# Optimization experiments

Hardware: AMD Instinct MI355X
Metric: run time of the kernel (lower is better)

## Reference

```python
import jax, jax.numpy as jnp
import numpy as np

H = 4
N = 1024
E = 4096
LE = 16384
FN = 128
FE = 64
FNO = 128
FEO = 64


def _lin(x, W, b):
    # torch nn.Linear: y = x @ W.T + b, W is [out, in]
    return x @ W.T + b


def setup_inputs() -> dict:
    key = jax.random.key(0)
    ks = jax.random.split(key, 24)
    s = 0.05
    inp = {}
    inp["node_inputs"] = jax.random.normal(ks[0], (N, FN), jnp.float32)
    inp["edge_inputs"] = jax.random.normal(ks[1], (E, FE), jnp.float32)
    inp["src"] = jax.random.randint(ks[2], (E,), 0, N, jnp.int32)
    inp["dst"] = jax.random.randint(ks[3], (E,), 0, N, jnp.int32)
    inp["lg_src"] = jax.random.randint(ks[4], (LE,), 0, E, jnp.int32)
    inp["lg_dst"] = jax.random.randint(ks[5], (LE,), 0, E, jnp.int32)
    # projection linear weights (torch Linear layout [out, in])
    inp["nqW"] = jax.random.normal(ks[6], (H * FN, FN), jnp.float32) * s
    inp["nqb"] = jax.random.normal(ks[7], (H * FN,), jnp.float32) * s
    inp["nkW"] = jax.random.normal(ks[8], (H, FN), jnp.float32) * s
    inp["nkb"] = jax.random.normal(ks[9], (H,), jnp.float32) * s
    inp["nvW"] = jax.random.normal(ks[10], (H * FN, FN), jnp.float32) * s
    inp["nvb"] = jax.random.normal(ks[11], (H * FN,), jnp.float32) * s
    inp["eqW"] = jax.random.normal(ks[12], (H * FE, FE), jnp.float32) * s
    inp["eqb"] = jax.random.normal(ks[13], (H * FE,), jnp.float32) * s
    inp["ekW"] = jax.random.normal(ks[14], (H, FE), jnp.float32) * s
    inp["ekb"] = jax.random.normal(ks[15], (H,), jnp.float32) * s
    inp["evW"] = jax.random.normal(ks[16], (H * FE, FE), jnp.float32) * s
    inp["evb"] = jax.random.normal(ks[17], (H * FE,), jnp.float32) * s
    # convolution output linears
    inp["ncW"] = jax.random.normal(ks[18], (FNO, FN), jnp.float32) * s
    inp["ncb"] = jax.random.normal(ks[19], (FNO,), jnp.float32) * s
    inp["ecW"] = jax.random.normal(ks[20], (FEO, FE), jnp.float32) * s
    inp["ecb"] = jax.random.normal(ks[21], (FEO,), jnp.float32) * s
    return inp


def reference(node_inputs, edge_inputs, src, dst, lg_src, lg_dst,
              nqW, nqb, nkW, nkb, nvW, nvb,
              eqW, eqb, ekW, ekb, evW, evb,
              ncW, ncb, ecW, ecb):
    n, fn = node_inputs.shape
    e, fe = edge_inputs.shape
    # per-head Q/K/V projections; .view(H, -1, F) == row-major reshape
    nq = _lin(node_inputs, nqW, nqb).reshape(H, -1, fn)   # [H,N,FN]
    nk = _lin(node_inputs, nkW, nkb).reshape(H, -1, 1)    # [H,N,1]
    nv = _lin(node_inputs, nvW, nvb).reshape(H, -1, fn)   # [H,N,FN]
    eq = _lin(edge_inputs, eqW, eqb).reshape(H, -1, fe)   # [H,E,FE]
    ek = _lin(edge_inputs, ekW, ekb).reshape(H, -1, 1)    # [H,E,1]
    ev = _lin(edge_inputs, evW, evb).reshape(H, -1, fe)   # [H,E,FE]
    # self attention: softmax(Q @ Q^T @ K, dim=1); associate as Q @ (Q^T K)
    node_sa = jax.nn.softmax(nq @ (jnp.swapaxes(nq, -1, -2) @ nk), axis=1)  # [H,N,1]
    edge_sa = jax.nn.softmax(eq @ (jnp.swapaxes(eq, -1, -2) @ ek), axis=1)  # [H,E,1]
    # vectorized edge-indexed scatter of attention scores into dense projections
    node_proj = jnp.zeros((H, n, n), node_inputs.dtype).at[:, src, dst].set(edge_sa[:, :, 0])
    conn = dst[lg_src]  # g.find_edges(source)[1]: destination node of edge lg_src
    edge_proj = jnp.zeros((H, e, e), edge_inputs.dtype).at[:, lg_src, lg_dst].set(node_sa[:, conn, 0])
    # dense adjacency matrices
    A = jnp.zeros((n, n), node_inputs.dtype).at[src, dst].set(1.0)
    Alg = jnp.zeros((e, e), edge_inputs.dtype).at[lg_src, lg_dst].set(1.0)
    # 'sum' aggregation: (attn_proj * A) @ value, then Linear + relu
    node_out = jax.nn.relu(_lin((node_proj * A) @ nv, ncW, ncb))   # [H,N,FNO]
    edge_out = jax.nn.relu(_lin((edge_proj * Alg) @ ev, ecW, ecb)) # [H,E,FEO]
    return (node_out, edge_out)
```

## Files before the change

kernel.cpp:

```cpp
#include <hip/hip_runtime.h>

#define H_ 4
#define N_ 1024
#define E_ 4096
#define LE_ 16384
#define FN_ 128
#define FE_ 64
#define CAP_ 32

struct P {
  const float *Xn, *Xe;
  const int *src, *dst, *lgs, *lgd;
  const float *nqW, *nqb, *nkW, *nkb, *nvW, *nvb;
  const float *eqW, *eqb, *ekW, *ekb, *evW, *evb;
  const float *ncW, *ncb, *ecW, *ecb;
  float *out;
  float *NV, *EV, *nsa, *esa, *nagg, *eagg;
  int *cntN, *cntE, *listN, *listE;
};

template<int K, bool RELU>
__device__ void gemm_tile(const float* __restrict__ X, const float* __restrict__ W,
                          const float* __restrict__ b, float* __restrict__ C,
                          int O, int r0, int o0, float* smem, int t) {
  float* Xs = smem;
  float* Ws = smem + 2048;
  const int tn = t & 15, tm = t >> 4;
  float acc[4][4] = {};
  for (int k0 = 0; k0 < K; k0 += 32) {
#pragma unroll
    for (int ph = 0; ph < 2; ++ph) {
      int i4 = t + ph * 256;
      int m = i4 >> 3;
      int k4 = (i4 & 7) << 2;
      int m4 = m >> 2, ml = m & 3;
      float4 vx = *(const float4*)&X[(r0 + m) * K + k0 + k4];
      float4 vw = *(const float4*)&W[(o0 + m) * K + k0 + k4];
      Xs[(k4 + 0) * 64 + ((m4 ^ ((k4 + 0) & 15)) << 2) + ml] = vx.x;
      Xs[(k4 + 1) * 64 + ((m4 ^ ((k4 + 1) & 15)) << 2) + ml] = vx.y;
      Xs[(k4 + 2) * 64 + ((m4 ^ ((k4 + 2) & 15)) << 2) + ml] = vx.z;
      Xs[(k4 + 3) * 64 + ((m4 ^ ((k4 + 3) & 15)) << 2) + ml] = vx.w;
      Ws[(k4 + 0) * 64 + ((m4 ^ ((k4 + 0) & 15)) << 2) + ml] = vw.x;
      Ws[(k4 + 1) * 64 + ((m4 ^ ((k4 + 1) & 15)) << 2) + ml] = vw.y;
      Ws[(k4 + 2) * 64 + ((m4 ^ ((k4 + 2) & 15)) << 2) + ml] = vw.z;
      Ws[(k4 + 3) * 64 + ((m4 ^ ((k4 + 3) & 15)) << 2) + ml] = vw.w;
    }
    __syncthreads();
#pragma unroll
    for (int k = 0; k < 32; ++k) {
      float4 a = *(const float4*)&Xs[k * 64 + ((tm ^ (k & 15)) << 2)];
      float4 b4 = *(const float4*)&Ws[k * 64 + ((tn ^ (k & 15)) << 2)];
      acc[0][0] += a.x * b4.x; acc[0][1] += a.x * b4.y; acc[0][2] += a.x * b4.z; acc[0][3] += a.x * b4.w;
      acc[1][0] += a.y * b4.x; acc[1][1] += a.y * b4.y; acc[1][2] += a.y * b4.z; acc[1][3] += a.y * b4.w;
      acc[2][0] += a.z * b4.x; acc[2][1] += a.z * b4.y; acc[2][2] += a.z * b4.z; acc[2][3] += a.z * b4.w;
      acc[3][0] += a.w * b4.x; acc[3][1] += a.w * b4.y; acc[3][2] += a.w * b4.z; acc[3][3] += a.w * b4.w;
    }
    __syncthreads();
  }
  float4 bv = *(const float4*)&b[o0 + tn * 4];
#pragma unroll
  for (int i = 0; i < 4; ++i) {
    float4 o;
    o.x = acc[i][0] + bv.x; o.y = acc[i][1] + bv.y;
    o.z = acc[i][2] + bv.z; o.w = acc[i][3] + bv.w;
    if (RELU) {
      o.x = fmaxf(o.x, 0.f); o.y = fmaxf(o.y, 0.f);
      o.z = fmaxf(o.z, 0.f); o.w = fmaxf(o.w, 0.f);
    }
    *(float4*)&C[(r0 + tm * 4 + i) * O + o0 + tn * 4] = o;
  }
}

__global__ __launch_bounds__(1024) void kA(P p) {
  __shared__ float S[16384];
  const int tid = threadIdx.x, bid = blockIdx.x;

  if (bid < 96) {
    int st = tid >> 8, tt = tid & 255;
    float* sm = S + st * 4096;
    if (bid < 32) {
      int T = bid * 4 + st;
      gemm_tile<128, false>(p.Xn, p.nvW, p.nvb, p.NV, 512, (T >> 3) * 64, (T & 7) * 64, sm, tt);
    } else {
      int T2 = (bid - 32) * 4 + st;
      gemm_tile<64, false>(p.Xe, p.evW, p.evb, p.EV, 256, (T2 >> 2) * 64, (T2 & 3) * 64, sm, tt);
    }
    return;
  }
  if (bid >= 104) {
    int idx = (bid - 104) * 1024 + tid;
    if (idx < E_) {
      int e = idx, s = p.src[e], d = p.dst[e];
      int pos = atomicAdd(&p.cntN[s], 1);
      p.listN[s * CAP_ + ((unsigned)pos & (CAP_ - 1))] = (d << 12) | e;
    } else {
      int l = idx - E_, j = p.lgs[l], c = p.lgd[l];
      int pos = atomicAdd(&p.cntE[j], 1);
      p.listE[j * CAP_ + ((unsigned)pos & (CAP_ - 1))] = (c << 14) | l;
    }
    return;
  }

  float4* accs = (float4*)S;
  float* sc    = S + 4096;
  float* knel  = S + 8192;
  float* red   = S + 12288;
  float* ys    = S + 13312;
  float* ts    = S + 13824;
  float* zs    = S + 13952;
  float* ds    = S + 14480;
  float* sig   = S + 14484;

  if (bid < 100) {
    const int h = bid - 96;
    const int r0 = h * 256;
    {
      int rl = tid >> 2, c = tid & 3;
      const float4* x4 = (const float4*)(p.Xn + (r0 + rl) * FN_);
      const float4* w4 = (const float4*)(p.nkW + c * FN_);
      float acc = p.nkb[c];
      for (int k = 0; k < 32; ++k) {
        float4 x = x4[k], w = w4[k];
        acc += x.x * w.x + x.y * w.y + x.z * w.z + x.w * w.w;
      }
      knel[rl * 4 + c] = acc;
    }
    __syncthreads();
    {
      int g = tid & 127, q = tid >> 7;
      float a0 = 0, a1 = 0, a2 = 0, a3 = 0;
      for (int jj = 0; jj < 32; ++jj) {
        int rl = q * 32 + jj;
        float x = p.Xn[(r0 + rl) * FN_ + g];
        float4 k = ((float4*)knel)[rl];
        a0 += x * k.x; a1 += x * k.y; a2 += x * k.z; a3 += x * k.w;
      }
      accs[tid] = make_float4(a0, a1, a2, a3);
    }
    __syncthreads();
    for (int off = 512; off >= 128; off >>= 1) {
      if (tid < off) {
        float4 a = accs[tid], b = accs[tid + off];
        accs[tid] = make_float4(a.x + b.x, a.y + b.y, a.z + b.z, a.w + b.w);
      }
      __syncthreads();
    }
    if (tid < 128) {
      float4 a = accs[tid];
      ys[tid * 4 + 0] = a.x; ys[tid * 4 + 1] = a.y;
      ys[tid * 4 + 2] = a.z; ys[tid * 4 + 3] = a.w;
    }
    if (tid >= 128 && tid < 160) {
      int t2 = tid - 128, c = t2 & 3, part = t2 >> 2;
      float s = 0.f;
      for (int j = 0; j < 32; ++j) s += knel[(part * 32 + j) * 4 + c];
      red[t2] = s;
    }
    __syncthreads();
    if (tid < 4) { float s = 0.f; for (int q = 0; q < 8; ++q) s += red[q * 4 + tid]; sig[tid] = s; }
    __syncthreads();
    if (tid < 512) {
      const float4* w4 = (const float4*)(p.nqW + tid * FN_);
      int c = tid >> 7;
      float s = 0.f;
      for (int g4 = 0; g4 < 32; ++g4) {
        float4 w = w4[g4];
        s += w.x * ys[(g4 * 4 + 0) * 4 + c] + w.y * ys[(g4 * 4 + 1) * 4 + c]
           + w.z * ys[(g4 * 4 + 2) * 4 + c] + w.w * ys[(g4 * 4 + 3) * 4 + c];
      }
      red[tid] = s;
    }
    __syncthreads();
    if (tid < 128) {
      float s = red[tid] + red[128 + tid] + red[256 + tid] + red[384 + tid];
      float bb = 0.f;
      for (int c = 0; c < 4; ++c) bb += p.nqb[c * 128 + tid] * sig[c];
      ts[tid] = s + bb;
    }
    __syncthreads();
    if (tid < 512) {
      int c = tid >> 7, g = tid & 127;
      float s = 0.f;
      for (int f = 0; f < 128; ++f) s += p.nqW[(c * 128 + f) * 128 + g] * ts[f];
      zs[c * 132 + g] = s;
    }
    if (tid >= 512 && tid < 516) {
      int c = tid - 512;
      float s = 0.f;
      for (int f = 0; f < 128; ++f) s += p.nqb[c * 128 + f] * ts[f];
      ds[c] = s;
    }
    __syncthreads();
    float scv;
    {
      int c = tid & 3, j = tid >> 2;
      const float4* x4 = (const float4*)(p.Xn + (r0 + j) * FN_);
      const float* z = zs + c * 132;
      float s = ds[c];
      for (int g4 = 0; g4 < 32; ++g4) {
        float4 x = x4[g4];
        s += x.x * z[g4 * 4] + x.y * z[g4 * 4 + 1] + x.z * z[g4 * 4 + 2] + x.w * z[g4 * 4 + 3];
      }
      scv = s;
    }
    red[tid] = scv;
    __syncthreads();
    for (int off = 512; off > 0; off >>= 1) {
      if (tid < off) red[tid] = fmaxf(red[tid], red[tid + off]);
      __syncthreads();
    }
    float m = red[0];
    __syncthreads();
    float e = expf(scv - m);
    red[tid] = e;
    __syncthreads();
    for (int off = 512; off > 0; off >>= 1) {
      if (tid < off) red[tid] += red[tid + off];
      __syncthreads();
    }
    p.nsa[h * N_ + tid] = e / red[0];
  } else {
    const int h = bid - 100;
    const int r0 = h * 1024;
    {
      const float4* x4 = (const float4*)(p.Xe + (r0 + tid) * FE_);
      const float4* w0 = (const float4*)(p.ekW + 0 * FE_);
      const float4* w1 = (const float4*)(p.ekW + 1 * FE_);
      const float4* w2 = (const float4*)(p.ekW + 2 * FE_);
      const float4* w3 = (const float4*)(p.ekW + 3 * FE_);
      float a0 = p.ekb[0], a1 = p.ekb[1], a2 = p.ekb[2], a3 = p.ekb[3];
      for (int k = 0; k < 16; ++k) {
        float4 x = x4[k];
        float4 u0 = w0[k], u1 = w1[k], u2 = w2[k], u3 = w3[k];
        a0 += x.x * u0.x + x.y * u0.y + x.z * u0.z + x.w * u0.w;
        a1 += x.x * u1.x + x.y * u1.y + x.z * u1.z + x.w * u1.w;
        a2 += x.x * u2.x + x.y * u2.y + x.z * u2.z + x.w * u2.w;
        a3 += x.x * u3.x + x.y * u3.y + x.z * u3.z + x.w * u3.w;
      }
      ((float4*)knel)[tid] = make_float4(a0, a1, a2, a3);
    }
    __syncthreads();
    {
      int g = tid & 63, q = tid >> 6;
      float a0 = 0, a1 = 0, a2 = 0, a3 = 0;
      for (int jj = 0; jj < 64; ++jj) {
        int rl = q * 64 + jj;
        float x = p.Xe[(r0 + rl) * FE_ + g];
        float4 k = ((float4*)knel)[rl];
        a0 += x * k.x; a1 += x * k.y; a2 += x * k.z; a3 += x * k.w;
      }
      accs[tid] = make_float4(a0, a1, a2, a3);
    }
    __syncthreads();
    for (int off = 512; off >= 64; off >>= 1) {
      if (tid < off) {
        float4 a = accs[tid], b = accs[tid + off];
        accs[tid] = make_float4(a.x + b.x, a.y + b.y, a.z + b.z, a.w + b.w);
      }
      __syncthreads();
    }
    if (tid < 64) {
      float4 a = accs[tid];
      ys[tid * 4 + 0] = a.x; ys[tid * 4 + 1] = a.y;
      ys[tid * 4 + 2] = a.z; ys[tid * 4 + 3] = a.w;
    }
    if (tid >= 128 && tid < 160) {
      int t2 = tid - 128, c = t2 & 3, part = t2 >> 2;
      float s = 0.f;
      for (int j = 0; j < 128; ++j) s += knel[(part * 128 + j) * 4 + c];
      red[t2] = s;
    }
    __syncthreads();
    if (tid < 4) { float s = 0.f; for (int q = 0; q < 8; ++q) s += red[q * 4 + tid]; sig[tid] = s; }
    __syncthreads();
    if (tid < 256) {
      const float4* w4 = (const float4*)(p.eqW + tid * FE_);
      int c = tid >> 6;
      float s = 0.f;
      for (int g4 = 0; g4 < 16; ++g4) {
        float4 w = w4[g4];
        s += w.x * ys[(g4 * 4 + 0) * 4 + c] + w.y * ys[(g4 * 4 + 1) * 4 + c]
           + w.z * ys[(g4 * 4 + 2) * 4 + c] + w.w * ys[(g4 * 4 + 3) * 4 + c];
      }
      red[tid] = s;
    }
    __syncthreads();
    if (tid < 64) {
      float s = red[tid] + red[64 + tid] + red[128 + tid] + red[192 + tid];
      float bb = 0.f;
      for (int c = 0; c < 4; ++c) bb += p.eqb[c * 64 + tid] * sig[c];
      ts[tid] = s + bb;
    }
    __syncthreads();
    if (tid < 256) {
      int c = tid >> 6, g = tid & 63;
      float s = 0.f;
      for (int f = 0; f < 64; ++f) s += p.eqW[(c * 64 + f) * 64 + g] * ts[f];
      zs[c * 132 + g] = s;
    }
    if (tid >= 256 && tid < 260) {
      int c = tid - 256;
      float s = 0.f;
      for (int f = 0; f < 64; ++f) s += p.eqb[c * 64 + f] * ts[f];
      ds[c] = s;
    }
    __syncthreads();
    float s4[4];
    {
      const float4* x4 = (const float4*)(p.Xe + (r0 + tid) * FE_);
      s4[0] = ds[0]; s4[1] = ds[1]; s4[2] = ds[2]; s4[3] = ds[3];
      for (int g4 = 0; g4 < 16; ++g4) {
        float4 x = x4[g4];
#pragma unroll
        for (int c = 0; c < 4; ++c) {
          const float* z = zs + c * 132 + g4 * 4;
          s4[c] += x.x * z[0] + x.y * z[1] + x.z * z[2] + x.w * z[3];
        }
      }
    }
    float lm = fmaxf(fmaxf(s4[0], s4[1]), fmaxf(s4[2], s4[3]));
    red[tid] = lm;
    __syncthreads();
    for (int off = 512; off > 0; off >>= 1) {
      if (tid < off) red[tid] = fmaxf(red[tid], red[tid + off]);
      __syncthreads();
    }
    float m = red[0];
    __syncthreads();
    float e0 = expf(s4[0] - m), e1 = expf(s4[1] - m);
    float e2 = expf(s4[2] - m), e3 = expf(s4[3] - m);
    red[tid] = e0 + e1 + e2 + e3;
    __syncthreads();
    for (int off = 512; off > 0; off >>= 1) {
      if (tid < off) red[tid] += red[tid + off];
      __syncthreads();
    }
    float inv = 1.f / red[0];
    ((float4*)(p.esa + h * E_))[tid] = make_float4(e0 * inv, e1 * inv, e2 * inv, e3 * inv);
  }
}

__global__ __launch_bounds__(256) void kB_gather(P p) {
  int idx = blockIdx.x * 256 + threadIdx.x;
  if (idx < N_ * 32) {
    unsigned base = (unsigned)p.cntN[N_];
    int s = idx >> 5, f4 = idx & 31;
    int deg = min((int)((unsigned)p.cntN[s] - base), CAP_);
    const int* lst = p.listN + s * CAP_;
    float4 acc[H_];
#pragma unroll
    for (int h = 0; h < H_; ++h) acc[h] = make_float4(0.f, 0.f, 0.f, 0.f);
    for (int i = 0; i < deg; ++i) {
      int pk = lst[(base + i) & (CAP_ - 1)];
      int d = pk >> 12, e = pk & (E_ - 1);
      bool win = true;
      for (int k = 0; k < deg; ++k) {
        int pk2 = lst[(base + k) & (CAP_ - 1)];
        if ((pk2 >> 12) == d && pk2 > pk) win = false;
      }
      if (!win) continue;
#pragma unroll
      for (int h = 0; h < H_; ++h) {
        float a = p.esa[h * E_ + e];
        float4 v = ((const float4*)(p.NV + h * (N_ * FN_) + d * FN_))[f4];
        acc[h].x += a * v.x; acc[h].y += a * v.y;
        acc[h].z += a * v.z; acc[h].w += a * v.w;
      }
    }
#pragma unroll
    for (int h = 0; h < H_; ++h)
      ((float4*)(p.nagg + h * (N_ * FN_) + s * FN_))[f4] = acc[h];
  } else {
    idx -= N_ * 32;
    unsigned base = (unsigned)p.cntE[E_];
    int j = idx >> 4, f4 = idx & 15;
    int deg = min((int)((unsigned)p.cntE[j] - base), CAP_);
    const int* lst = p.listE + j * CAP_;
    float4 acc[H_];
#pragma unroll
    for (int h = 0; h < H_; ++h) acc[h] = make_float4(0.f, 0.f, 0.f, 0.f);
    for (int i = 0; i < deg; ++i) {
      int pk = lst[(base + i) & (CAP_ - 1)];
      int c = pk >> 14;
      bool win = true;
      for (int k = 0; k < deg; ++k) {
        int pk2 = lst[(base + k) & (CAP_ - 1)];
        if ((pk2 >> 14) == c && pk2 > pk) win = false;
      }
      if (!win) continue;
#pragma unroll
      for (int h = 0; h < H_; ++h) {
        float4 v = ((const float4*)(p.EV + h * (E_ * FE_) + c * FE_))[f4];
        acc[h].x += v.x; acc[h].y += v.y; acc[h].z += v.z; acc[h].w += v.w;
      }
    }
    int cn = p.dst[j];
#pragma unroll
    for (int h = 0; h < H_; ++h) {
      float a = p.nsa[h * N_ + cn];
      ((float4*)(p.eagg + h * (E_ * FE_) + j * FE_))[f4] =
          make_float4(a * acc[h].x, a * acc[h].y, a * acc[h].z, a * acc[h].w);
    }
  }
}

__global__ __launch_bounds__(256) void kC_out(P p) {
  __shared__ float smem[4096];
  const int t = threadIdx.x, bid = blockIdx.x;
  if (bid < 128)
    gemm_tile<128, true>(p.nagg, p.ncW, p.ncb, p.out, 128, (bid >> 1) * 64, (bid & 1) * 64, smem, t);
  else {
    int T2 = bid - 128;
    gemm_tile<64, true>(p.eagg, p.ecW, p.ecb, p.out + (size_t)H_ * N_ * 128, 64, T2 * 64, 0, smem, t);
  }
}

extern "C" void kernel_launch(void* const* d_in, const int* in_sizes, int n_in,
                              void* d_out, int out_size, void* d_ws, size_t ws_size,
                              hipStream_t stream) {
  P p;
  p.Xn  = (const float*)d_in[0];
  p.Xe  = (const float*)d_in[1];
  p.src = (const int*)d_in[2];
  p.dst = (const int*)d_in[3];
  p.lgs = (const int*)d_in[4];
  p.lgd = (const int*)d_in[5];
  p.nqW = (const float*)d_in[6];  p.nqb = (const float*)d_in[7];
  p.nkW = (const float*)d_in[8];  p.nkb = (const float*)d_in[9];
  p.nvW = (const float*)d_in[10]; p.nvb = (const float*)d_in[11];
  p.eqW = (const float*)d_in[12]; p.eqb = (const float*)d_in[13];
  p.ekW = (const float*)d_in[14]; p.ekb = (const float*)d_in[15];
  p.evW = (const float*)d_in[16]; p.evb = (const float*)d_in[17];
  p.ncW = (const float*)d_in[18]; p.ncb = (const float*)d_in[19];
  p.ecW = (const float*)d_in[20]; p.ecb = (const float*)d_in[21];
  p.out = (float*)d_out;

  float* f = (float*)d_ws;
  p.NV   = f; f += N_ * H_ * FN_;
  p.EV   = f; f += E_ * H_ * FE_;
  p.nsa  = f; f += H_ * N_;
  p.esa  = f; f += H_ * E_;
  p.nagg = f; f += H_ * N_ * FN_;
  p.eagg = f; f += H_ * E_ * FE_;
  p.cntN = (int*)f; f += N_ + 1;
  p.cntE = (int*)f; f += E_ + 1;
  p.listN = (int*)f; f += N_ * CAP_;
  p.listE = (int*)f; f += E_ * CAP_;

  kA<<<124, 1024, 0, stream>>>(p);
  kB_gather<<<384, 256, 0, stream>>>(p);
  kC_out<<<384, 256, 0, stream>>>(p);
}
```

Baseline: 185.2 us.

## Fuse sparse gather into output GEMM and precompute deduplicated adjacency lists

The aggregation step that wrote nagg/eagg to global memory is folded into the output-linear kernel. Each block now gathers its 64 rows straight into shared memory and runs the GEMM from there, which removes an intermediate write and read. The O(deg^2) duplicate-edge resolution now runs once per row into compacted lists, instead of once per feature lane. The V projections move out of the attention kernel into a separate 256-thread kernel with more blocks. In exchange, the gather in the output kernel has each thread hold 32 accumulators and read uncoalesced rows, which may hurt occupancy, and a one-thread-per-row dedup pass is added.

Result: faster. 180.6 us (-2.5%).

```diff
diff --git a/kernel.cpp b/kernel.cpp
--- a/kernel.cpp
+++ b/kernel.cpp
@@ -15,8 +15,11 @@
   const float *eqW, *eqb, *ekW, *ekb, *evW, *evb;
   const float *ncW, *ncb, *ecW, *ecb;
   float *out;
-  float *NV, *EV, *nsa, *esa, *nagg, *eagg;
-  int *cntN, *cntE, *listN, *listE;
+  float *NV, *EV, *nsa, *esa;
+  int *cntN, *cntE;
+  int *listN, *listE;
+  int *listNc, *listEc;
+  int *degN, *degE;
 };
 
 template<int K, bool RELU>
@@ -71,24 +74,12 @@
   }
 }
 
-__global__ __launch_bounds__(1024) void kA(P p) {
+__global__ __launch_bounds__(1024) void A_attn(P p) {
   __shared__ float S[16384];
   const int tid = threadIdx.x, bid = blockIdx.x;
 
-  if (bid < 96) {
-    int st = tid >> 8, tt = tid & 255;
-    float* sm = S + st * 4096;
-    if (bid < 32) {
-      int T = bid * 4 + st;
-      gemm_tile<128, false>(p.Xn, p.nvW, p.nvb, p.NV, 512, (T >> 3) * 64, (T & 7) * 64, sm, tt);
-    } else {
-      int T2 = (bid - 32) * 4 + st;
-      gemm_tile<64, false>(p.Xe, p.evW, p.evb, p.EV, 256, (T2 >> 2) * 64, (T2 & 3) * 64, sm, tt);
-    }
-    return;
-  }
-  if (bid >= 104) {
-    int idx = (bid - 104) * 1024 + tid;
+  if (bid >= 8) {
+    int idx = (bid - 8) * 1024 + tid;
     if (idx < E_) {
       int e = idx, s = p.src[e], d = p.dst[e];
       int pos = atomicAdd(&p.cntN[s], 1);
@@ -111,8 +102,8 @@
   float* ds    = S + 14480;
   float* sig   = S + 14484;
 
-  if (bid < 100) {
-    const int h = bid - 96;
+  if (bid < 4) {
+    const int h = bid;
     const int r0 = h * 256;
     {
       int rl = tid >> 2, c = tid & 3;
@@ -220,14 +211,14 @@
     }
     p.nsa[h * N_ + tid] = e / red[0];
   } else {
-    const int h = bid - 100;
+    const int h = bid - 4;
     const int r0 = h * 1024;
     {
       const float4* x4 = (const float4*)(p.Xe + (r0 + tid) * FE_);
-      const float4* w0 = (const float4*)(p.ekW + 0 * FE_);
-      const float4* w1 = (const float4*)(p.ekW + 1 * FE_);
-      const float4* w2 = (const float4*)(p.ekW + 2 * FE_);
-      const float4* w3 = (const float4*)(p.ekW + 3 * FE_);
+      const float4* w0 = (const float4*)(p.ekW);
+      const float4* w1 = (const float4*)(p.ekW + 64);
+      const float4* w2 = (const float4*)(p.ekW + 128);
+      const float4* w3 = (const float4*)(p.ekW + 192);
       float a0 = p.ekb[0], a1 = p.ekb[1], a2 = p.ekb[2], a3 = p.ekb[3];
       for (int k = 0; k < 16; ++k) {
         float4 x = x4[k];
@@ -340,78 +331,192 @@
   }
 }
 
-__global__ __launch_bounds__(256) void kB_gather(P p) {
-  int idx = blockIdx.x * 256 + threadIdx.x;
-  if (idx < N_ * 32) {
-    unsigned base = (unsigned)p.cntN[N_];
-    int s = idx >> 5, f4 = idx & 31;
-    int deg = min((int)((unsigned)p.cntN[s] - base), CAP_);
-    const int* lst = p.listN + s * CAP_;
-    float4 acc[H_];
-#pragma unroll
-    for (int h = 0; h < H_; ++h) acc[h] = make_float4(0.f, 0.f, 0.f, 0.f);
-    for (int i = 0; i < deg; ++i) {
-      int pk = lst[(base + i) & (CAP_ - 1)];
-      int d = pk >> 12, e = pk & (E_ - 1);
-      bool win = true;
-      for (int k = 0; k < deg; ++k) {
-        int pk2 = lst[(base + k) & (CAP_ - 1)];
-        if ((pk2 >> 12) == d && pk2 > pk) win = false;
-      }
-      if (!win) continue;
-#pragma unroll
-      for (int h = 0; h < H_; ++h) {
-        float a = p.esa[h * E_ + e];
-        float4 v = ((const float4*)(p.NV + h * (N_ * FN_) + d * FN_))[f4];
-        acc[h].x += a * v.x; acc[h].y += a * v.y;
-        acc[h].z += a * v.z; acc[h].w += a * v.w;
-      }
-    }
-#pragma unroll
-    for (int h = 0; h < H_; ++h)
-      ((float4*)(p.nagg + h * (N_ * FN_) + s * FN_))[f4] = acc[h];
+__global__ __launch_bounds__(256) void B_vproj(P p) {
+  __shared__ float S[4096];
+  const int t = threadIdx.x, bid = blockIdx.x;
+  if (bid < 128) {
+    gemm_tile<128, false>(p.Xn, p.nvW, p.nvb, p.NV, 512, (bid >> 3) * 64, (bid & 7) * 64, S, t);
+  } else if (bid < 384) {
+    int T2 = bid - 128;
+    gemm_tile<64, false>(p.Xe, p.evW, p.evb, p.EV, 256, (T2 >> 2) * 64, (T2 & 3) * 64, S, t);
   } else {
-    idx -= N_ * 32;
-    unsigned base = (unsigned)p.cntE[E_];
-    int j = idx >> 4, f4 = idx & 15;
-    int deg = min((int)((unsigned)p.cntE[j] - base), CAP_);
-    const int* lst = p.listE + j * CAP_;
-    float4 acc[H_];
-#pragma unroll
-    for (int h = 0; h < H_; ++h) acc[h] = make_float4(0.f, 0.f, 0.f, 0.f);
-    for (int i = 0; i < deg; ++i) {
-      int pk = lst[(base + i) & (CAP_ - 1)];
-      int c = pk >> 14;
-      bool win = true;
-      for (int k = 0; k < deg; ++k) {
-        int pk2 = lst[(base + k) & (CAP_ - 1)];
-        if ((pk2 >> 14) == c && pk2 > pk) win = false;
-      }
-      if (!win) continue;
-#pragma unroll
-      for (int h = 0; h < H_; ++h) {
-        float4 v = ((const float4*)(p.EV + h * (E_ * FE_) + c * FE_))[f4];
-        acc[h].x += v.x; acc[h].y += v.y; acc[h].z += v.z; acc[h].w += v.w;
-      }
-    }
-    int cn = p.dst[j];
-#pragma unroll
-    for (int h = 0; h < H_; ++h) {
-      float a = p.nsa[h * N_ + cn];
-      ((float4*)(p.eagg + h * (E_ * FE_) + j * FE_))[f4] =
-          make_float4(a * acc[h].x, a * acc[h].y, a * acc[h].z, a * acc[h].w);
+    int idx = (bid - 384) * 256 + t;
+    if (idx < N_) {
+      int s = idx;
+      unsigned base = (unsigned)p.cntN[N_];
+      int deg = min((int)((unsigned)p.cntN[s] - base), CAP_);
+      const int* lst = p.listN + s * CAP_;
+      int* dstl = p.listNc + s * CAP_;
+      int w = 0;
+      for (int i = 0; i < deg; ++i) {
+        int pk = lst[(base + i) & (CAP_ - 1)];
+        bool win = true;
+        for (int k2 = 0; k2 < deg; ++k2) {
+          int pk2 = lst[(base + k2) & (CAP_ - 1)];
+          if ((pk2 >> 12) == (pk >> 12) && pk2 > pk) win = false;
+        }
+        if (win) dstl[w++] = pk;
+      }
+      p.degN[s] = w;
+    } else {
+      int j = idx - N_;
+      unsigned base = (unsigned)p.cntE[E_];
+      int deg = min((int)((unsigned)p.cntE[j] - base), CAP_);
+      const int* lst = p.listE + j * CAP_;
+      int* dstl = p.listEc + j * CAP_;
+      int w = 0;
+      for (int i = 0; i < deg; ++i) {
+        int pk = lst[(base + i) & (CAP_ - 1)];
+        bool win = true;
+        for (int k2 = 0; k2 < deg; ++k2) {
+          int pk2 = lst[(base + k2) & (CAP_ - 1)];
+          if ((pk2 >> 14) == (pk >> 14) && pk2 > pk) win = false;
+        }
+        if (win) dstl[w++] = pk;
+      }
+      p.degE[j] = w;
     }
   }
 }
 
-__global__ __launch_bounds__(256) void kC_out(P p) {
-  __shared__ float smem[4096];
+__global__ __launch_bounds__(256) void C_out(P p) {
+  __shared__ float S[10240];
   const int t = threadIdx.x, bid = blockIdx.x;
-  if (bid < 128)
-    gemm_tile<128, true>(p.nagg, p.ncW, p.ncb, p.out, 128, (bid >> 1) * 64, (bid & 1) * 64, smem, t);
-  else {
-    int T2 = bid - 128;
-    gemm_tile<64, true>(p.eagg, p.ecW, p.ecb, p.out + (size_t)H_ * N_ * 128, 64, T2 * 64, 0, smem, t);
+  const int tn = t & 15, tm = t >> 4;
+  float* Xs = S;
+
+  if (bid < 128) {
+    float* Ws = S + 8192;
+    int rt = bid >> 1, o0 = (bid & 1) * 64;
+    int r0 = rt * 64;
+    int h = r0 >> 10, s0 = r0 & (N_ - 1);
+    {
+      int m = t >> 2, g0 = (t & 3) * 32;
+      int m4 = m >> 2, ml = m & 3;
+      int s = s0 + m;
+      int deg = p.degN[s];
+      const int* lst = p.listNc + s * CAP_;
+      float acc[32];
+#pragma unroll
+      for (int c = 0; c < 32; ++c) acc[c] = 0.f;
+      for (int i = 0; i < deg; ++i) {
+        int pk = lst[i];
+        int e = pk & (E_ - 1), d = pk >> 12;
+        float a = p.esa[h * E_ + e];
+        const float4* v4 = (const float4*)(p.NV + h * (N_ * FN_) + d * FN_ + g0);
+#pragma unroll
+        for (int c4 = 0; c4 < 8; ++c4) {
+          float4 v = v4[c4];
+          acc[c4 * 4 + 0] += a * v.x; acc[c4 * 4 + 1] += a * v.y;
+          acc[c4 * 4 + 2] += a * v.z; acc[c4 * 4 + 3] += a * v.w;
+        }
+      }
+#pragma unroll
+      for (int c = 0; c < 32; ++c) {
+        int k = g0 + c;
+        Xs[k * 64 + ((m4 ^ (k & 15)) << 2) + ml] = acc[c];
+      }
+    }
+    float accO[4][4] = {};
+    for (int k0 = 0; k0 < 128; k0 += 32) {
+      __syncthreads();
+#pragma unroll
+      for (int ph = 0; ph < 2; ++ph) {
+        int i4 = t + ph * 256;
+        int m = i4 >> 3, k4 = (i4 & 7) << 2;
+        int m4 = m >> 2, ml = m & 3;
+        float4 vw = *(const float4*)&p.ncW[(o0 + m) * 128 + k0 + k4];
+        Ws[(k4 + 0) * 64 + ((m4 ^ ((k4 + 0) & 15)) << 2) + ml] = vw.x;
+        Ws[(k4 + 1) * 64 + ((m4 ^ ((k4 + 1) & 15)) << 2) + ml] = vw.y;
+        Ws[(k4 + 2) * 64 + ((m4 ^ ((k4 + 2) & 15)) << 2) + ml] = vw.z;
+        Ws[(k4 + 3) * 64 + ((m4 ^ ((k4 + 3) & 15)) << 2) + ml] = vw.w;
+      }
+      __syncthreads();
+#pragma unroll
+      for (int k = 0; k < 32; ++k) {
+        int ka = k0 + k;
+        float4 a = *(const float4*)&Xs[ka * 64 + ((tm ^ (ka & 15)) << 2)];
+        float4 b4 = *(const float4*)&Ws[k * 64 + ((tn ^ (k & 15)) << 2)];
+        accO[0][0] += a.x * b4.x; accO[0][1] += a.x * b4.y; accO[0][2] += a.x * b4.z; accO[0][3] += a.x * b4.w;
+        accO[1][0] += a.y * b4.x; accO[1][1] += a.y * b4.y; accO[1][2] += a.y * b4.z; accO[1][3] += a.y * b4.w;
+        accO[2][0] += a.z * b4.x; accO[2][1] += a.z * b4.y; accO[2][2] += a.z * b4.z; accO[2][3] += a.z * b4.w;
+        accO[3][0] += a.w * b4.x; accO[3][1] += a.w * b4.y; accO[3][2] += a.w * b4.z; accO[3][3] += a.w * b4.w;
+      }
+    }
+    float4 bv = *(const float4*)&p.ncb[o0 + tn * 4];
+#pragma unroll
+    for (int i = 0; i < 4; ++i) {
+      float4 o;
+      o.x = fmaxf(accO[i][0] + bv.x, 0.f); o.y = fmaxf(accO[i][1] + bv.y, 0.f);
+      o.z = fmaxf(accO[i][2] + bv.z, 0.f); o.w = fmaxf(accO[i][3] + bv.w, 0.f);
+      *(float4*)&p.out[(r0 + tm * 4 + i) * 128 + o0 + tn * 4] = o;
+    }
+  } else {
+    float* Ws = S + 4096;
+    int T = bid - 128;
+    int r0 = T * 64;
+    int h = r0 >> 12, j0 = r0 & (E_ - 1);
+    {
+      int m = t >> 2, g0 = (t & 3) * 16;
+      int m4 = m >> 2, ml = m & 3;
+      int j = j0 + m;
+      int deg = p.degE[j];
+      const int* lst = p.listEc + j * CAP_;
+      float acc[16];
+#pragma unroll
+      for (int c = 0; c < 16; ++c) acc[c] = 0.f;
+      for (int i = 0; i < deg; ++i) {
+        int c = lst[i] >> 14;
+        const float4* v4 = (const float4*)(p.EV + h * (E_ * FE_) + c * FE_ + g0);
+#pragma unroll
+        for (int c4 = 0; c4 < 4; ++c4) {
+          float4 v = v4[c4];
+          acc[c4 * 4 + 0] += v.x; acc[c4 * 4 + 1] += v.y;
+          acc[c4 * 4 + 2] += v.z; acc[c4 * 4 + 3] += v.w;
+        }
+      }
+      float a = p.nsa[h * N_ + p.dst[j]];
+#pragma unroll
+      for (int c = 0; c < 16; ++c) {
+        int k = g0 + c;
+        Xs[k * 64 + ((m4 ^ (k & 15)) << 2) + ml] = a * acc[c];
+      }
+    }
+    float accO[4][4] = {};
+    for (int k0 = 0; k0 < 64; k0 += 32) {
+      __syncthreads();
+#pragma unroll
+      for (int ph = 0; ph < 2; ++ph) {
+        int i4 = t + ph * 256;
+        int m = i4 >> 3, k4 = (i4 & 7) << 2;
+        int m4 = m >> 2, ml = m & 3;
+        float4 vw = *(const float4*)&p.ecW[m * 64 + k0 + k4];
+        Ws[(k4 + 0) * 64 + ((m4 ^ ((k4 + 0) & 15)) << 2) + ml] = vw.x;
+        Ws[(k4 + 1) * 64 + ((m4 ^ ((k4 + 1) & 15)) << 2) + ml] = vw.y;
+        Ws[(k4 + 2) * 64 + ((m4 ^ ((k4 + 2) & 15)) << 2) + ml] = vw.z;
+        Ws[(k4 + 3) * 64 + ((m4 ^ ((k4 + 3) & 15)) << 2) + ml] = vw.w;
+      }
+      __syncthreads();
+#pragma unroll
+      for (int k = 0; k < 32; ++k) {
+        int ka = k0 + k;
+        float4 a = *(const float4*)&Xs[ka * 64 + ((tm ^ (ka & 15)) << 2)];
+        float4 b4 = *(const float4*)&Ws[k * 64 + ((tn ^ (k & 15)) << 2)];
+        accO[0][0] += a.x * b4.x; accO[0][1] += a.x * b4.y; accO[0][2] += a.x * b4.z; accO[0][3] += a.x * b4.w;
+        accO[1][0] += a.y * b4.x; accO[1][1] += a.y * b4.y; accO[1][2] += a.y * b4.z; accO[1][3] += a.y * b4.w;
+        accO[2][0] += a.z * b4.x; accO[2][1] += a.z * b4.y; accO[2][2] += a.z * b4.z; accO[2][3] += a.z * b4.w;
+        accO[3][0] += a.w * b4.x; accO[3][1] += a.w * b4.y; accO[3][2] += a.w * b4.z; accO[3][3] += a.w * b4.w;
+      }
+    }
+    float4 bv = *(const float4*)&p.ecb[tn * 4];
+    float* outE = p.out + (size_t)H_ * N_ * 128;
+#pragma unroll
+    for (int i = 0; i < 4; ++i) {
+      float4 o;
+      o.x = fmaxf(accO[i][0] + bv.x, 0.f); o.y = fmaxf(accO[i][1] + bv.y, 0.f);
+      o.z = fmaxf(accO[i][2] + bv.z, 0.f); o.w = fmaxf(accO[i][3] + bv.w, 0.f);
+      *(float4*)&outE[(r0 + tm * 4 + i) * 64 + tn * 4] = o;
+    }
   }
 }
 
@@ -436,18 +541,20 @@
   p.out = (float*)d_out;
 
   float* f = (float*)d_ws;
-  p.NV   = f; f += N_ * H_ * FN_;
-  p.EV   = f; f += E_ * H_ * FE_;
-  p.nsa  = f; f += H_ * N_;
-  p.esa  = f; f += H_ * E_;
-  p.nagg = f; f += H_ * N_ * FN_;
-  p.eagg = f; f += H_ * E_ * FE_;
-  p.cntN = (int*)f; f += N_ + 1;
-  p.cntE = (int*)f; f += E_ + 1;
+  p.NV    = f; f += N_ * H_ * FN_;
+  p.EV    = f; f += E_ * H_ * FE_;
+  p.nsa   = f; f += H_ * N_;
+  p.esa   = f; f += H_ * E_;
+  p.cntN  = (int*)f; f += N_ + 1;
+  p.cntE  = (int*)f; f += E_ + 1;
   p.listN = (int*)f; f += N_ * CAP_;
   p.listE = (int*)f; f += E_ * CAP_;
-
-  kA<<<124, 1024, 0, stream>>>(p);
-  kB_gather<<<384, 256, 0, stream>>>(p);
-  kC_out<<<384, 256, 0, stream>>>(p);
+  p.listNc = (int*)f; f += N_ * CAP_;
+  p.listEc = (int*)f; f += E_ * CAP_;
+  p.degN  = (int*)f; f += N_;
+  p.degE  = (int*)f; f += E_;
+
+  A_attn<<<28, 1024, 0, stream>>>(p);
+  B_vproj<<<404, 256, 0, stream>>>(p);
+  C_out<<<384, 256, 0, stream>>>(p);
 }
```
